# Optimization experiments

Measured on AMD Instinct MI355X. Metric: run time of the kernel, lower is better.

## Reference

```python
import jax, jax.numpy as jnp
import numpy as np

H = 1024      # hidden_size
NH = 16       # num_attention_heads
HD = H // NH  # attention_head_size = 64
FF = 4096     # intermediate_size
EPS = 1e-5


def setup_inputs() -> dict:
    key = jax.random.key(0)
    ks = jax.random.split(key, 16)
    B, S = 8, 512
    s = lambda d: 1.0 / np.sqrt(d)
    return {
        "hidden_states": jax.random.normal(ks[0], (B, S, H), jnp.float32),
        "attention_mask": jnp.zeros((B, 1, 1, S), jnp.float32),  # additive mask
        "wq": jax.random.normal(ks[1], (H, H), jnp.float32) * s(H),
        "bq": jnp.zeros((H,), jnp.float32),
        "wk": jax.random.normal(ks[2], (H, H), jnp.float32) * s(H),
        "bk": jnp.zeros((H,), jnp.float32),
        "wv": jax.random.normal(ks[3], (H, H), jnp.float32) * s(H),
        "bv": jnp.zeros((H,), jnp.float32),
        "wo": jax.random.normal(ks[4], (H, H), jnp.float32) * s(H),
        "bo": jnp.zeros((H,), jnp.float32),
        "ln1_g": jnp.ones((H,), jnp.float32),
        "ln1_b": jnp.zeros((H,), jnp.float32),
        "wi": jax.random.normal(ks[5], (H, FF), jnp.float32) * s(H),
        "bi": jnp.zeros((FF,), jnp.float32),
        "wo2": jax.random.normal(ks[6], (FF, H), jnp.float32) * s(FF),
        "bo2": jnp.zeros((H,), jnp.float32),
        "ln2_g": jnp.ones((H,), jnp.float32),
        "ln2_b": jnp.zeros((H,), jnp.float32),
    }


def _layer_norm(x, g, b):
    mu = jnp.mean(x, axis=-1, keepdims=True)
    var = jnp.mean(jnp.square(x - mu), axis=-1, keepdims=True)
    return (x - mu) * jax.lax.rsqrt(var + EPS) * g + b


def reference(hidden_states, attention_mask, wq, bq, wk, bk, wv, bv,
              wo, bo, ln1_g, ln1_b, wi, bi, wo2, bo2, ln2_g, ln2_b):
    B, S, _ = hidden_states.shape
    split = lambda x: x.reshape(B, S, NH, HD).transpose(0, 2, 1, 3)  # [B,NH,S,HD]
    q = split(hidden_states @ wq + bq)
    k = split(hidden_states @ wk + bk)
    v = split(hidden_states @ wv + bv)
    # scaled dot-product attention with additive mask (dropout = eval identity)
    scores = jnp.einsum("bhqd,bhkd->bhqk", q, k) / np.sqrt(HD)
    scores = scores + attention_mask
    probs = jax.nn.softmax(scores, axis=-1)
    ctx = jnp.einsum("bhqk,bhkd->bhqd", probs, v)
    ctx = ctx.transpose(0, 2, 1, 3).reshape(B, S, H)
    # RobertaSelfOutput: dense + residual + LayerNorm
    attn_out = _layer_norm(ctx @ wo + bo + hidden_states, ln1_g, ln1_b)
    # FFN: intermediate (gelu) + output dense + residual + LayerNorm
    inter = jax.nn.gelu(attn_out @ wi + bi, approximate=False)
    layer_out = _layer_norm(inter @ wo2 + bo2 + attn_out, ln2_g, ln2_b)
    return layer_out
```

## Files before the change

### kernel.cpp

```cpp
#include <hip/hip_runtime.h>
#include <math.h>

#define DI __device__ __forceinline__

typedef unsigned short u16;
typedef __attribute__((ext_vector_type(8))) u16 u16x8;
typedef __attribute__((ext_vector_type(4))) u16 u16x4;
typedef __attribute__((ext_vector_type(8))) __bf16 bf16x8;
typedef __attribute__((ext_vector_type(4))) float f32x4;

typedef const __attribute__((address_space(1))) unsigned int g_u32;
typedef __attribute__((address_space(3))) unsigned int l_u32;

DI float bf2f(u16 u) {
  unsigned v = ((unsigned)u) << 16;
  float f; __builtin_memcpy(&f, &v, 4); return f;
}
DI u16 f2bf(float f) {
  unsigned u; __builtin_memcpy(&u, &f, 4);
  u += 0x7fff + ((u >> 16) & 1);
  return (u16)(u >> 16);
}
DI f32x4 mfma16(bf16x8 a, bf16x8 b, f32x4 c) {
  return __builtin_amdgcn_mfma_f32_16x16x32_bf16(a, b, c, 0, 0, 0);
}
DI void gl16(const void* g, const u16* lds) {
  __builtin_amdgcn_global_load_lds((g_u32*)g, (l_u32*)lds, 16, 0, 0);
}

__global__ __launch_bounds__(256) void cvt_bf16_k(const float* __restrict__ in,
                                                  u16* __restrict__ out, int n) {
  int i = (blockIdx.x * 256 + threadIdx.x) * 8;
  if (i >= n) return;
  float4 a = *(const float4*)(in + i);
  float4 b = *(const float4*)(in + i + 4);
  u16x8 o;
  o[0] = f2bf(a.x); o[1] = f2bf(a.y); o[2] = f2bf(a.z); o[3] = f2bf(a.w);
  o[4] = f2bf(b.x); o[5] = f2bf(b.y); o[6] = f2bf(b.z); o[7] = f2bf(b.w);
  *(u16x8*)(out + i) = o;
}

__global__ __launch_bounds__(256) void tcvt_k(const float* __restrict__ in,
                                              u16* __restrict__ out, int K, int N) {
  __shared__ float tile[32][33];
  int n0 = blockIdx.x * 32, k0 = blockIdx.y * 32;
  int tx = threadIdx.x & 31, ty = threadIdx.x >> 5;
  #pragma unroll
  for (int i = 0; i < 4; i++) {
    int kr = ty + i * 8;
    tile[kr][tx] = in[(size_t)(k0 + kr) * N + n0 + tx];
  }
  __syncthreads();
  #pragma unroll
  for (int i = 0; i < 4; i++) {
    int nr = ty + i * 8;
    out[(size_t)(n0 + nr) * K + k0 + tx] = f2bf(tile[tx][nr]);
  }
}

__global__ __launch_bounds__(256) void pack_bias_k(const float* __restrict__ b0,
                                                   const float* __restrict__ b1,
                                                   const float* __restrict__ b2,
                                                   float* __restrict__ out) {
  int i = blockIdx.x * 256 + threadIdx.x;
  float v = (i < 1024) ? b0[i] : (i < 2048 ? b1[i - 1024] : b2[i - 2048]);
  out[i] = v;
}

template<int EPI>
__global__ __launch_bounds__(256) void gemm_bt_k(const u16* __restrict__ A,
                                                 const u16* __restrict__ Bt,
                                                 const float* __restrict__ bias,
                                                 const void* __restrict__ resid,
                                                 u16* __restrict__ out,
                                                 int M, int N, int K) {
  __shared__ __align__(16) u16 As[128 * 64];
  __shared__ __align__(16) u16 Bs[128 * 64];
  const int tid = threadIdx.x;
  const int lane = tid & 63, wid = tid >> 6;
  const int wm = (wid >> 1) * 64, wn = (wid & 1) * 64;
  const int bm = blockIdx.y * 128, bn = blockIdx.x * 128;
  const int r15 = lane & 15, kg = lane >> 4;

  const int srow = lane >> 3;
  const int scolb = (lane & 7) << 4;

  f32x4 acc[4][4];
  #pragma unroll
  for (int i = 0; i < 4; i++)
    #pragma unroll
    for (int j = 0; j < 4; j++) acc[i][j] = (f32x4){0.f, 0.f, 0.f, 0.f};

  for (int kt = 0; kt < K; kt += 64) {
    #pragma unroll
    for (int c = 0; c < 4; c++) {
      int chunk = (c << 2) | wid;
      int row = (chunk << 3) + srow;
      gl16((const char*)A + ((size_t)(bm + row) * K + kt) * 2 + scolb,
           (const u16*)((const char*)As + (chunk << 10)));
      gl16((const char*)Bt + ((size_t)(bn + row) * K + kt) * 2 + scolb,
           (const u16*)((const char*)Bs + (chunk << 10)));
    }
    __syncthreads();
    #pragma unroll
    for (int ks = 0; ks < 2; ks++) {
      bf16x8 af[4], bfr[4];
      #pragma unroll
      for (int i = 0; i < 4; i++)
        af[i] = *(const bf16x8*)&As[(wm + i * 16 + r15) * 64 + ks * 32 + kg * 8];
      #pragma unroll
      for (int i = 0; i < 4; i++)
        bfr[i] = *(const bf16x8*)&Bs[(wn + i * 16 + r15) * 64 + ks * 32 + kg * 8];
      #pragma unroll
      for (int i = 0; i < 4; i++)
        #pragma unroll
        for (int j = 0; j < 4; j++)
          acc[i][j] = mfma16(af[i], bfr[j], acc[i][j]);
    }
    __syncthreads();
  }

  #pragma unroll
  for (int i = 0; i < 4; i++) {
    int row0 = bm + wm + i * 16 + kg * 4;
    #pragma unroll
    for (int j = 0; j < 4; j++) {
      int col = bn + wn + j * 16 + r15;
      float bv = bias[col];
      #pragma unroll
      for (int q = 0; q < 4; q++) {
        int row = row0 + q;
        float v = acc[i][j][q] + bv;
        if (EPI == 1) v += ((const float*)resid)[(size_t)row * N + col];
        if (EPI == 2) v = 0.5f * v * (1.0f + erff(v * 0.70710678118f));
        if (EPI == 3) v += bf2f(((const u16*)resid)[(size_t)row * N + col]);
        out[(size_t)row * N + col] = f2bf(v);
      }
    }
  }
}

__global__ __launch_bounds__(256) void attn_k(const u16* __restrict__ QKV,
                                              const float* __restrict__ mask,
                                              u16* __restrict__ ctx) {
  __shared__ __align__(16) u16 sQ[32 * 72];
  __shared__ __align__(16) u16 sK[64 * 72];
  __shared__ __align__(16) u16 sVt[64 * 72];
  __shared__ __align__(16) u16 sS[32 * 520];
  __shared__ float sSum[32];
  const int t = threadIdx.x, lane = t & 63, wid = t >> 6;
  const int qb = blockIdx.x, h = blockIdx.y, b = blockIdx.z;
  const int r15 = lane & 15, kg = lane >> 4;
  const int mg = wid >> 1, half = wid & 1;
  const size_t qoff = (size_t)h * 64;
  const size_t koff = 1024 + qoff, voff = 2048 + qoff;

  {
    int row = t >> 3, d0 = (t & 7) * 8;
    *(u16x8*)&sQ[row * 72 + d0] =
        *(const u16x8*)&QKV[((size_t)(b * 512 + qb * 32 + row)) * 3072 + qoff + d0];
  }

  for (int kt = 0; kt < 8; ++kt) {
    int row = t >> 2, d0 = (t & 3) * 16;
    const u16* src = &QKV[((size_t)(b * 512 + kt * 64 + row)) * 3072 + koff + d0];
    *(u16x8*)&sK[row * 72 + d0] = *(const u16x8*)src;
    *(u16x8*)&sK[row * 72 + d0 + 8] = *(const u16x8*)(src + 8);
    __syncthreads();
    bf16x8 qf0 = *(const bf16x8*)&sQ[(mg * 16 + r15) * 72 + kg * 8];
    bf16x8 qf1 = *(const bf16x8*)&sQ[(mg * 16 + r15) * 72 + 32 + kg * 8];
    #pragma unroll
    for (int n2 = 0; n2 < 2; n2++) {
      int nt = half * 2 + n2;
      f32x4 sacc = (f32x4){0.f, 0.f, 0.f, 0.f};
      sacc = mfma16(qf0, *(const bf16x8*)&sK[(nt * 16 + r15) * 72 + kg * 8], sacc);
      sacc = mfma16(qf1, *(const bf16x8*)&sK[(nt * 16 + r15) * 72 + 32 + kg * 8], sacc);
      int col = kt * 64 + nt * 16 + r15;
      float mv = mask[b * 512 + col];
      #pragma unroll
      for (int q = 0; q < 4; q++) {
        int rl = mg * 16 + kg * 4 + q;
        sS[rl * 520 + col] = f2bf(sacc[q] * 0.125f + mv);
      }
    }
    __syncthreads();
  }

  {
    int row = t >> 3, seg = t & 7;
    float mx = -1e30f;
    for (int j = 0; j < 64; j++)
      mx = fmaxf(mx, bf2f(sS[row * 520 + seg * 64 + j]));
    mx = fmaxf(mx, __shfl_xor(mx, 1));
    mx = fmaxf(mx, __shfl_xor(mx, 2));
    mx = fmaxf(mx, __shfl_xor(mx, 4));
    float sum = 0.f;
    for (int j = 0; j < 64; j++) {
      int idx = row * 520 + seg * 64 + j;
      float p = __expf(bf2f(sS[idx]) - mx);
      sum += p;
      sS[idx] = f2bf(p);
    }
    sum += __shfl_xor(sum, 1);
    sum += __shfl_xor(sum, 2);
    sum += __shfl_xor(sum, 4);
    if (seg == 0) sSum[row] = sum;
  }
  __syncthreads();

  f32x4 pacc[2];
  pacc[0] = (f32x4){0.f, 0.f, 0.f, 0.f};
  pacc[1] = (f32x4){0.f, 0.f, 0.f, 0.f};
  for (int vt = 0; vt < 8; ++vt) {
    int rowk = t >> 2, d0 = (t & 3) * 16;
    const u16* src = &QKV[((size_t)(b * 512 + vt * 64 + rowk)) * 3072 + voff + d0];
    u16x8 v0 = *(const u16x8*)src;
    u16x8 v1 = *(const u16x8*)(src + 8);
    #pragma unroll
    for (int e = 0; e < 8; e++) {
      sVt[(d0 + e) * 72 + rowk] = v0[e];
      sVt[(d0 + 8 + e) * 72 + rowk] = v1[e];
    }
    __syncthreads();
    bf16x8 pf0 = *(const bf16x8*)&sS[(mg * 16 + r15) * 520 + vt * 64 + kg * 8];
    bf16x8 pf1 = *(const bf16x8*)&sS[(mg * 16 + r15) * 520 + vt * 64 + 32 + kg * 8];
    #pragma unroll
    for (int n2 = 0; n2 < 2; n2++) {
      int dcol = half * 32 + n2 * 16;
      pacc[n2] = mfma16(pf0, *(const bf16x8*)&sVt[(dcol + r15) * 72 + kg * 8], pacc[n2]);
      pacc[n2] = mfma16(pf1, *(const bf16x8*)&sVt[(dcol + r15) * 72 + 32 + kg * 8], pacc[n2]);
    }
    __syncthreads();
  }
  #pragma unroll
  for (int n2 = 0; n2 < 2; n2++) {
    int d = half * 32 + n2 * 16 + r15;
    #pragma unroll
    for (int q = 0; q < 4; q++) {
      int rl = mg * 16 + kg * 4 + q;
      float v = pacc[n2][q] / sSum[rl];
      ctx[((size_t)(b * 512 + qb * 32 + rl)) * 1024 + qoff + d] = f2bf(v);
    }
  }
}

template<int OUTF32>
__global__ __launch_bounds__(256) void ln_k(const u16* __restrict__ in,
                                            const float* __restrict__ g,
                                            const float* __restrict__ be,
                                            void* __restrict__ out) {
  int row = blockIdx.x, t = threadIdx.x;
  const u16* rp = in + (size_t)row * 1024 + t * 4;
  u16x4 raw = *(const u16x4*)rp;
  float x[4];
  #pragma unroll
  for (int i = 0; i < 4; i++) x[i] = bf2f(raw[i]);
  float s = x[0] + x[1] + x[2] + x[3];
  float q = x[0]*x[0] + x[1]*x[1] + x[2]*x[2] + x[3]*x[3];
  #pragma unroll
  for (int off = 32; off; off >>= 1) {
    s += __shfl_down(s, off);
    q += __shfl_down(q, off);
  }
  __shared__ float rs_[4], rq_[4];
  int wid = t >> 6, lane = t & 63;
  if (!lane) { rs_[wid] = s; rq_[wid] = q; }
  __syncthreads();
  float S1 = rs_[0] + rs_[1] + rs_[2] + rs_[3];
  float S2 = rq_[0] + rq_[1] + rq_[2] + rq_[3];
  float mu = S1 * (1.0f / 1024.0f);
  float inv = rsqrtf(S2 * (1.0f / 1024.0f) - mu * mu + 1e-5f);
  #pragma unroll
  for (int i = 0; i < 4; i++) {
    int c = t * 4 + i;
    float y = (x[i] - mu) * inv * g[c] + be[c];
    if (OUTF32) ((float*)out)[(size_t)row * 1024 + c] = y;
    else        ((u16*)out)[(size_t)row * 1024 + c] = f2bf(y);
  }
}

extern "C" void kernel_launch(void* const* d_in, const int* in_sizes, int n_in,
                              void* d_out, int out_size, void* d_ws, size_t ws_size,
                              hipStream_t stream) {
  const float* hidden = (const float*)d_in[0];
  const float* mask   = (const float*)d_in[1];
  const float* wq  = (const float*)d_in[2];  const float* bq  = (const float*)d_in[3];
  const float* wk  = (const float*)d_in[4];  const float* bk  = (const float*)d_in[5];
  const float* wv  = (const float*)d_in[6];  const float* bv  = (const float*)d_in[7];
  const float* wo  = (const float*)d_in[8];  const float* bo  = (const float*)d_in[9];
  const float* ln1g = (const float*)d_in[10]; const float* ln1b = (const float*)d_in[11];
  const float* wi  = (const float*)d_in[12]; const float* bi  = (const float*)d_in[13];
  const float* wo2 = (const float*)d_in[14]; const float* bo2 = (const float*)d_in[15];
  const float* ln2g = (const float*)d_in[16]; const float* ln2b = (const float*)d_in[17];

  char* ws = (char*)d_ws;
  size_t off = 0;
  auto alloc = [&](size_t elems) -> u16* {
    u16* p = (u16*)(ws + off);
    off += ((elems * 2 + 255) & ~(size_t)255);
    return p;
  };
  u16* Xb    = alloc(4194304);
  u16* WqkvT = alloc(3145728);
  u16* WoT   = alloc(1048576);
  u16* WiT   = alloc(4194304);
  u16* Wo2T  = alloc(4194304);
  u16* QKVb  = alloc(12582912);
  u16* Ctx   = alloc(4194304);
  u16* AD    = alloc(4194304);
  u16* AO    = alloc(4194304);
  u16* Inter = alloc(16777216);
  u16* FD    = alloc(4194304);
  float* bqkv = (float*)(ws + off); off += 3072 * 4;

  cvt_bf16_k<<<2048, 256, 0, stream>>>(hidden, Xb, 4194304);
  tcvt_k<<<dim3(32, 32),  256, 0, stream>>>(wq,  WqkvT,                1024, 1024);
  tcvt_k<<<dim3(32, 32),  256, 0, stream>>>(wk,  WqkvT + 1024 * 1024,  1024, 1024);
  tcvt_k<<<dim3(32, 32),  256, 0, stream>>>(wv,  WqkvT + 2048 * 1024,  1024, 1024);
  tcvt_k<<<dim3(32, 32),  256, 0, stream>>>(wo,  WoT,  1024, 1024);
  tcvt_k<<<dim3(128, 32), 256, 0, stream>>>(wi,  WiT,  1024, 4096);
  tcvt_k<<<dim3(32, 128), 256, 0, stream>>>(wo2, Wo2T, 4096, 1024);
  pack_bias_k<<<12, 256, 0, stream>>>(bq, bk, bv, bqkv);

  gemm_bt_k<0><<<dim3(24, 32), 256, 0, stream>>>(Xb, WqkvT, bqkv, nullptr, QKVb, 4096, 3072, 1024);

  attn_k<<<dim3(16, 16, 8), 256, 0, stream>>>(QKVb, mask, Ctx);

  gemm_bt_k<1><<<dim3(8, 32), 256, 0, stream>>>(Ctx, WoT, bo, hidden, AD, 4096, 1024, 1024);
  ln_k<0><<<4096, 256, 0, stream>>>(AD, ln1g, ln1b, AO);
  gemm_bt_k<2><<<dim3(32, 32), 256, 0, stream>>>(AO, WiT, bi, nullptr, Inter, 4096, 4096, 1024);
  gemm_bt_k<3><<<dim3(8, 32), 256, 0, stream>>>(Inter, Wo2T, bo2, AO, FD, 4096, 1024, 4096);
  ln_k<1><<<4096, 256, 0, stream>>>(FD, ln2g, ln2b, d_out);
}
```

Baseline: 454.9 us.

## Double-buffer GEMM LDS tiles and remap blocks for XCD-aware L2 locality

The GEMM kernel now uses two LDS buffers so the global-to-LDS load of the next K tile is issued before computing on the current tile, leaving one barrier per iteration instead of two. It also remaps workgroup IDs so consecutive blocks on each XCD cover a band of up to 8 column tiles, which is meant to improve L2 reuse of the operands. LDS use doubles to 64KB per block, which may lower occupancy.

Result: slower. 491.0 us (+7.9%).

```diff
diff --git a/kernel.cpp b/kernel.cpp
--- a/kernel.cpp
+++ b/kernel.cpp
@@ -74,51 +74,74 @@
                                                  const void* __restrict__ resid,
                                                  u16* __restrict__ out,
                                                  int M, int N, int K) {
-  __shared__ __align__(16) u16 As[128 * 64];
-  __shared__ __align__(16) u16 Bs[128 * 64];
+  __shared__ __align__(16) u16 As[2][128 * 64];
+  __shared__ __align__(16) u16 Bs[2][128 * 64];
   const int tid = threadIdx.x;
   const int lane = tid & 63, wid = tid >> 6;
   const int wm = (wid >> 1) * 64, wn = (wid & 1) * 64;
-  const int bm = blockIdx.y * 128, bn = blockIdx.x * 128;
   const int r15 = lane & 15, kg = lane >> 4;
-
   const int srow = lane >> 3;
   const int scolb = (lane & 7) << 4;
 
+  const int GX = gridDim.x, GY = gridDim.y;
+  int nwg = GX * GY;
+  int orig = blockIdx.y * GX + blockIdx.x;
+  int q = nwg >> 3, r = nwg & 7;
+  int xcd = orig & 7, idx = orig >> 3;
+  int s = (xcd < r ? xcd * (q + 1) : r * (q + 1) + (xcd - r) * q) + idx;
+  int CG = (GX >= 8) ? 8 : GX;
+  int band = GY * CG;
+  int g = s / band, rem = s - g * band;
+  int by = rem / CG;
+  int bx = g * CG + (rem - by * CG);
+  const int bm = by * 128, bn = bx * 128;
+
   f32x4 acc[4][4];
   #pragma unroll
   for (int i = 0; i < 4; i++)
     #pragma unroll
     for (int j = 0; j < 4; j++) acc[i][j] = (f32x4){0.f, 0.f, 0.f, 0.f};
 
-  for (int kt = 0; kt < K; kt += 64) {
+  auto STAGE = [&](int buf, int kt) {
     #pragma unroll
     for (int c = 0; c < 4; c++) {
       int chunk = (c << 2) | wid;
       int row = (chunk << 3) + srow;
       gl16((const char*)A + ((size_t)(bm + row) * K + kt) * 2 + scolb,
-           (const u16*)((const char*)As + (chunk << 10)));
+           &As[buf][chunk << 9]);
       gl16((const char*)Bt + ((size_t)(bn + row) * K + kt) * 2 + scolb,
-           (const u16*)((const char*)Bs + (chunk << 10)));
-    }
-    __syncthreads();
+           &Bs[buf][chunk << 9]);
+    }
+  };
+  auto COMPUTE = [&](int buf) {
     #pragma unroll
     for (int ks = 0; ks < 2; ks++) {
       bf16x8 af[4], bfr[4];
       #pragma unroll
       for (int i = 0; i < 4; i++)
-        af[i] = *(const bf16x8*)&As[(wm + i * 16 + r15) * 64 + ks * 32 + kg * 8];
+        af[i] = *(const bf16x8*)&As[buf][(wm + i * 16 + r15) * 64 + ks * 32 + kg * 8];
       #pragma unroll
       for (int i = 0; i < 4; i++)
-        bfr[i] = *(const bf16x8*)&Bs[(wn + i * 16 + r15) * 64 + ks * 32 + kg * 8];
+        bfr[i] = *(const bf16x8*)&Bs[buf][(wn + i * 16 + r15) * 64 + ks * 32 + kg * 8];
       #pragma unroll
       for (int i = 0; i < 4; i++)
         #pragma unroll
         for (int j = 0; j < 4; j++)
           acc[i][j] = mfma16(af[i], bfr[j], acc[i][j]);
     }
-    __syncthreads();
-  }
+  };
+
+  const int nt = K >> 6;
+  STAGE(0, 0);
+  __syncthreads();
+  int cur = 0;
+  for (int t = 0; t + 1 < nt; ++t) {
+    STAGE(cur ^ 1, (t + 1) << 6);
+    COMPUTE(cur);
+    __syncthreads();
+    cur ^= 1;
+  }
+  COMPUTE(cur);
 
   #pragma unroll
   for (int i = 0; i < 4; i++) {
@@ -128,9 +151,9 @@
       int col = bn + wn + j * 16 + r15;
       float bv = bias[col];
       #pragma unroll
-      for (int q = 0; q < 4; q++) {
-        int row = row0 + q;
-        float v = acc[i][j][q] + bv;
+      for (int q2 = 0; q2 < 4; q2++) {
+        int row = row0 + q2;
+        float v = acc[i][j][q2] + bv;
         if (EPI == 1) v += ((const float*)resid)[(size_t)row * N + col];
         if (EPI == 2) v = 0.5f * v * (1.0f + erff(v * 0.70710678118f));
         if (EPI == 3) v += bf2f(((const u16*)resid)[(size_t)row * N + col]);
```
